# Kernel tuning notes

Hardware: AMD Instinct MI355X
Metric: run time of the kernel (lower is better)

Reference implementation:

```python
import jax, jax.numpy as jnp
import numpy as np

B, H, S, D = 2, 16, 2048, 64
MASK_NEG = 1e9


def setup_inputs() -> dict:
    key = jax.random.key(0)
    kq, kk, kv, km = jax.random.split(key, 4)
    Q = jax.random.normal(kq, (B, H, S, D), dtype=jnp.float32)
    K = jax.random.normal(kk, (B, H, S, D), dtype=jnp.float32)
    V = jax.random.normal(kv, (B, H, S, D), dtype=jnp.float32)
    # float 0/1 mask, broadcast over heads; 1 = masked-out position
    attn_mask = jax.random.randint(km, (B, 1, S, S), 0, 2).astype(jnp.float32)
    return {"Q": Q, "K": K, "V": V, "attn_mask": attn_mask}


def reference(Q, K, V, attn_mask):
    # scores: [B, H, S, S]
    attn_score = jnp.einsum('bhqd,bhkd->bhqk', Q, K)
    scale = jnp.sqrt(jnp.asarray(K.shape[-1], dtype=jnp.float32))
    attn_scale = attn_score / scale - MASK_NEG * attn_mask
    attn_prob = jax.nn.softmax(attn_scale, axis=-1)
    attn_out = jnp.einsum('bhqk,bhkd->bhqd', attn_prob, V)
    return attn_out
```

## Files before the change

kernel.cpp:

```cpp
#include <hip/hip_runtime.h>


#define S_LEN 2048
#define D_DIM 64
#define WPR   32
#define NIT   32

typedef __attribute__((ext_vector_type(8)))  short bf16x8;
typedef __attribute__((ext_vector_type(4)))  float f32x4;
typedef __attribute__((ext_vector_type(16))) float f32x16;
typedef unsigned uint2v __attribute__((ext_vector_type(2)));
typedef unsigned long long ull;

__device__ __forceinline__ f32x16 mfma32(bf16x8 a, bf16x8 b, f32x16 c) {
  return __builtin_amdgcn_mfma_f32_32x32x16_bf16(a, b, c, 0, 0, 0);
}
__device__ __forceinline__ f32x4 mfma16(bf16x8 a, bf16x8 b, f32x4 c) {
  return __builtin_amdgcn_mfma_f32_16x16x32_bf16(a, b, c, 0, 0, 0);
}
__device__ __forceinline__ unsigned short f2bf(float f) {
  unsigned u = __builtin_bit_cast(unsigned, f);
  unsigned r = u + 0x7FFFu + ((u >> 16) & 1u);
  return (unsigned short)(r >> 16);
}
__device__ __forceinline__ float bf2f(unsigned short s) {
  unsigned u = ((unsigned)s) << 16;
  return __builtin_bit_cast(float, u);
}
__device__ __forceinline__ unsigned packbf(float a, float b) {
  unsigned r;
  asm("v_cvt_pk_bf16_f32 %0, %1, %2" : "=v"(r) : "v"(a), "v"(b));
  return r;
}
__device__ __forceinline__ float fexp2(float x) {
#if __has_builtin(__builtin_amdgcn_exp2f)
  return __builtin_amdgcn_exp2f(x);
#else
  return exp2f(x);
#endif
}
__device__ __forceinline__ bool detect_bf16(const void* maskp) {
  const unsigned short* s = (const unsigned short*)maskp;
  unsigned short v = s[2 * (threadIdx.x & 63)];
  return __ballot(v == (unsigned short)0x3F80) != 0ull;
}
__device__ __forceinline__ int4 cvt_f8(const float* p) {
  float4 f0 = *(const float4*)p;
  float4 f1 = *(const float4*)(p + 4);
  int4 r;
  r.x = (int)packbf(f0.x, f0.y);
  r.y = (int)packbf(f0.z, f0.w);
  r.z = (int)packbf(f1.x, f1.y);
  r.w = (int)packbf(f1.z, f1.w);
  return r;
}
__device__ __forceinline__ void gl_lds16(const unsigned short* g, unsigned short* l) {
#if __has_builtin(__builtin_amdgcn_global_load_lds)
  __builtin_amdgcn_global_load_lds(
      (const __attribute__((address_space(1))) unsigned int*)g,
      (__attribute__((address_space(3))) unsigned int*)l, 16, 0, 0);
#else
  *(int4*)((char*)l + (threadIdx.x & 63) * 16) = *(const int4*)g;
#endif
}

#define C1 0.18033688011112042f
#define C2 1.4426950408889634e9f

#define SEG0 4096u
#define SEG1 2048u
#define SEG2 1024u
#define SEG3 2048u

__global__ __launch_bounds__(256) void prep_all(
    const void* __restrict__ M, const void* __restrict__ Kin,
    const void* __restrict__ Vin, const void* __restrict__ Qin,
    ull* __restrict__ bits, unsigned short* __restrict__ Kf,
    unsigned short* __restrict__ Vf, unsigned short* __restrict__ Qc) {
  __shared__ __align__(16) unsigned short T[64 * 72];
  const bool isb = detect_bf16(M);
  const unsigned bx = blockIdx.x;
  const int tid = threadIdx.x;

  if (bx < SEG0) {
    unsigned e0 = bx * 2048u + tid;
    #pragma unroll
    for (int j = 0; j < 8; ++j) {
      unsigned idx = e0 + (unsigned)j * 256u;
      bool on = isb ? (bf2f(((const unsigned short*)M)[idx]) > 0.5f)
                    : (((const float*)M)[idx] > 0.5f);
      ull bm = __ballot(on);
      if ((tid & 63) == 0) {
        unsigned c = idx & 2047u, r = (idx >> 11) & 2047u, bb = idx >> 22;
        bits[(((size_t)(bb * WPR + (c >> 6))) << 11) + r] = bm;
      }
    }
  } else if (bx < SEG0 + SEG1) {
    unsigned g = (bx - SEG0) * 256u + tid;
    unsigned lane = g & 63u, f = (g >> 6) & 7u, it = (g >> 9) & 31u, bh = g >> 14;
    unsigned t = f >> 2, dc = f & 3, hi = lane >> 5, l31 = lane & 31;
    size_t src = (size_t)bh * (S_LEN * D_DIM) +
                 (size_t)(it * 64 + t * 32 + l31) * D_DIM + dc * 16 + hi * 8;
    int4 out;
    if (isb) out = *(const int4*)((const unsigned short*)Kin + src);
    else     out = cvt_f8((const float*)Kin + src);
    *(int4*)&Kf[(size_t)g * 8] = out;
  } else if (bx < SEG0 + SEG1 + SEG2) {
    unsigned idx = bx - (SEG0 + SEG1);
    unsigned bh = idx >> 5, it = idx & 31u;
    {
      int k = tid >> 2, d0 = (tid & 3) * 16;
      size_t src = (size_t)bh * (S_LEN * D_DIM) + (size_t)(it * 64 + k) * D_DIM + d0;
      int4 a, c;
      if (isb) {
        const unsigned short* s = (const unsigned short*)Vin + src;
        a = *(const int4*)s; c = *(const int4*)(s + 8);
      } else {
        const float* s = (const float*)Vin + src;
        a = cvt_f8(s); c = cvt_f8(s + 8);
      }
      *(int4*)&T[k * 72 + d0] = a;
      *(int4*)&T[k * 72 + d0 + 8] = c;
    }
    __syncthreads();
    #pragma unroll
    for (int h = 0; h < 2; ++h) {
      int c = tid + h * 256;
      int lane = c & 63, f = c >> 6;
      int t = f >> 2, kc = (f >> 1) & 1, dt = f & 1;
      int hi = lane >> 5, l31 = lane & 31;
      unsigned short v[8];
      #pragma unroll
      for (int j = 0; j < 8; ++j)
        v[j] = T[(t * 32 + kc * 16 + hi * 8 + j) * 72 + dt * 32 + l31];
      *(int4*)&Vf[(((size_t)(bh * 32 + it)) * 8 + f) * 512 + lane * 8] = *(int4*)v;
    }
  } else {
    size_t i0 = ((size_t)(bx - (SEG0 + SEG1 + SEG2)) * 256 + tid) * 8;
    unsigned short v[8];
    if (isb) {
      *(int4*)v = *(const int4*)((const unsigned short*)Qin + i0);
      #pragma unroll
      for (int j = 0; j < 8; ++j) v[j] = f2bf(bf2f(v[j]) * C1);
    } else {
      const float* f = (const float*)Qin + i0;
      #pragma unroll
      for (int j = 0; j < 4; ++j)
        *((unsigned*)v + j) = packbf(f[2 * j] * C1, f[2 * j + 1] * C1);
    }
    *(int4*)&Qc[i0] = *(int4*)v;
  }
}

__global__ __launch_bounds__(256, 4) void attn_fast(
    const unsigned short* __restrict__ Qc, const unsigned short* __restrict__ Kf,
    const unsigned short* __restrict__ Vf, const ull* __restrict__ bits,
    const void* __restrict__ maskp, void* __restrict__ Op) {
  __shared__ __align__(16) unsigned short Stg[2][8][512];
  __shared__ float Ls[4][32];

  const bool isb = detect_bf16(maskp);
  const int tid  = threadIdx.x;
  const int wave = tid >> 6;
  const int lane = tid & 63;
  const int hi   = lane >> 5;
  const int l31  = lane & 31;
  const int id   = blockIdx.x;
  const int slot = id >> 3;
  const int bh   = (id & 7) * 4 + (slot & 3);
  const int qb   = slot >> 2;
  const int qbase = qb * 128 + wave * 32;
  const int b    = bh >> 4;
  const size_t base = (size_t)bh * S_LEN * D_DIM;
  const int xidx = ((lane ^ 32) & 63) * 4;

  bf16x8 qf[4];
  #pragma unroll
  for (int dc = 0; dc < 4; ++dc)
    qf[dc] = *(const bf16x8*)&Qc[base + (size_t)(qbase + l31) * D_DIM + dc * 16 + hi * 8];

  const unsigned short* Ksrc = Kf + (size_t)bh * 131072 + (size_t)wave * 512 + lane * 8;
  const unsigned short* Vsrc = Vf + (size_t)bh * 131072 + (size_t)wave * 512 + lane * 8;
  const size_t bitbase = ((size_t)(b * WPR) << 11) + (size_t)(qbase + l31);

  f32x16 acc_o[2];
  float ls0 = 0.f, ls1 = 0.f, ls2 = 0.f, ls3 = 0.f;
  #pragma unroll
  for (int r = 0; r < 16; ++r) { acc_o[0][r] = 0.f; acc_o[1][r] = 0.f; }

  gl_lds16(Ksrc, &Stg[0][wave][0]);
  gl_lds16(Vsrc, &Stg[0][4 + wave][0]);
  __syncthreads();

  ull wcur = 0;
  #pragma unroll 2
  for (int ks = 0; ks < 64; ++ks) {
    const int cur = ks & 1;
    if (ks < 63) {
      gl_lds16(Ksrc + (size_t)(ks + 1) * 2048, &Stg[cur ^ 1][wave][0]);
      gl_lds16(Vsrc + (size_t)(ks + 1) * 2048, &Stg[cur ^ 1][4 + wave][0]);
    }
    if (!(ks & 1)) wcur = bits[bitbase + ((size_t)(ks >> 1) << 11)];

    f32x16 sc;
    #pragma unroll
    for (int r = 0; r < 16; ++r) sc[r] = 0.f;
    #pragma unroll
    for (int dc = 0; dc < 4; ++dc) {
      bf16x8 kfr = *(const bf16x8*)&Stg[cur][dc][lane * 8];
      sc = mfma32(kfr, qf[dc], sc);
    }

    const unsigned wtv = (unsigned)((wcur >> (hi * 4)) >> (32 * (ks & 1)));

    float p[16];
    #pragma unroll
    for (int r = 0; r < 16; ++r) {
      float e = fexp2(sc[r]);
      unsigned bit = (wtv >> ((r & 3) + 8 * (r >> 2))) & 1u;
      p[r] = bit ? 0.0f : e;
    }
    ls0 += p[0] + p[4] + p[8]  + p[12];
    ls1 += p[1] + p[5] + p[9]  + p[13];
    ls2 += p[2] + p[6] + p[10] + p[14];
    ls3 += p[3] + p[7] + p[11] + p[15];

    #pragma unroll
    for (int kc = 0; kc < 2; ++kc) {
      unsigned pk0 = packbf(p[8 * kc + 0], p[8 * kc + 1]);
      unsigned pk1 = packbf(p[8 * kc + 2], p[8 * kc + 3]);
      unsigned pk2 = packbf(p[8 * kc + 4], p[8 * kc + 5]);
      unsigned pk3 = packbf(p[8 * kc + 6], p[8 * kc + 7]);
      uint4 d;
#if __has_builtin(__builtin_amdgcn_permlane32_swap)
      uint2v s02 = __builtin_amdgcn_permlane32_swap(pk0, pk2, false, false);
      uint2v s13 = __builtin_amdgcn_permlane32_swap(pk1, pk3, false, false);
      d.x = s02[0]; d.z = s02[1];
      d.y = s13[0]; d.w = s13[1];
#else
      unsigned x0 = (unsigned)__builtin_amdgcn_ds_bpermute(xidx, (int)pk0);
      unsigned x1 = (unsigned)__builtin_amdgcn_ds_bpermute(xidx, (int)pk1);
      unsigned x2 = (unsigned)__builtin_amdgcn_ds_bpermute(xidx, (int)pk2);
      unsigned x3 = (unsigned)__builtin_amdgcn_ds_bpermute(xidx, (int)pk3);
      d.x = hi ? x2 : pk0;
      d.y = hi ? x3 : pk1;
      d.z = hi ? pk2 : x0;
      d.w = hi ? pk3 : x1;
#endif
      bf16x8 pf = __builtin_bit_cast(bf16x8, d);
      #pragma unroll
      for (int dt = 0; dt < 2; ++dt) {
        bf16x8 vfr = *(const bf16x8*)&Stg[cur][4 + kc * 2 + dt][lane * 8];
        acc_o[dt] = mfma32(pf, vfr, acc_o[dt]);
      }
    }

    __syncthreads();
  }

  float lsum = (ls0 + ls1) + (ls2 + ls3);
  {
    int li = __builtin_bit_cast(int, lsum);
    float other = __builtin_bit_cast(float, __builtin_amdgcn_ds_bpermute(xidx, li));
    lsum += other;
  }
  if (hi == 0) Ls[wave][l31] = lsum;

  #pragma unroll
  for (int r = 0; r < 16; ++r) {
    int m = (r & 3) + 8 * (r >> 2) + 4 * hi;
    float inv = 1.0f / Ls[wave][m];
    float o0 = acc_o[0][r] * inv;
    float o1 = acc_o[1][r] * inv;
    size_t idx = base + (size_t)(qbase + m) * D_DIM + l31;
    if (isb) {
      ((unsigned short*)Op)[idx]      = f2bf(o0);
      ((unsigned short*)Op)[idx + 32] = f2bf(o1);
    } else {
      ((float*)Op)[idx]      = o0;
      ((float*)Op)[idx + 32] = o1;
    }
  }
}

__global__ __launch_bounds__(256, 2) void attn_fallback(
    const void* __restrict__ Qp, const void* __restrict__ Kp,
    const void* __restrict__ Vp, const void* __restrict__ maskp,
    void* __restrict__ Op) {
  __shared__ __align__(16) short QKlds[128 * 72];
  __shared__ __align__(16) short Vtlds[64 * 72];
  __shared__ __align__(16) short Plds2[128 * 72];

  const bool isb = detect_bf16(maskp);
  const int tid  = threadIdx.x;
  const int wave = tid >> 6;
  const int lane = tid & 63;
  const int l15  = lane & 15;
  const int quad = lane >> 4;
  const int q0   = blockIdx.x * 128;
  const int bh   = blockIdx.y;
  const int b    = bh >> 4;
  const size_t base = (size_t)bh * S_LEN * D_DIM;

  const short* Qs = (const short*)Qp; const float* Qf = (const float*)Qp;
  const short* Ks = (const short*)Kp; const float* Kf2 = (const float*)Kp;
  const short* Vs = (const short*)Vp; const float* Vf2 = (const float*)Vp;

  if (isb) {
    const short* Qg = Qs + base + (size_t)q0 * D_DIM;
    #pragma unroll
    for (int p = 0; p < 4; ++p) {
      int e = p * 2048 + tid * 8;
      *(int4*)&QKlds[(e >> 6) * 72 + (e & 63)] = *(const int4*)(Qg + e);
    }
  } else {
    const float* Qg = Qf + base + (size_t)q0 * D_DIM;
    #pragma unroll
    for (int p = 0; p < 4; ++p) {
      int e = p * 2048 + tid * 8;
      *(int4*)&QKlds[(e >> 6) * 72 + (e & 63)] = cvt_f8(Qg + e);
    }
  }
  __syncthreads();
  bf16x8 qf[2][2];
  #pragma unroll
  for (int mi = 0; mi < 2; ++mi)
    #pragma unroll
    for (int kt = 0; kt < 2; ++kt)
      qf[mi][kt] = *(const bf16x8*)&QKlds[(wave * 32 + mi * 16 + l15) * 72 + kt * 32 + quad * 8];
  __syncthreads();

  f32x4 acc_o[2][4];
  f32x4 acc_l[2];
  const f32x4 zero4 = {0.f, 0.f, 0.f, 0.f};
  #pragma unroll
  for (int mi = 0; mi < 2; ++mi) {
    acc_l[mi] = zero4;
    #pragma unroll
    for (int nt = 0; nt < 4; ++nt) acc_o[mi][nt] = zero4;
  }
  bf16x8 onesB;
  {
    short ov = (l15 == 0) ? (short)0x3F80 : (short)0;
    #pragma unroll
    for (int i = 0; i < 8; ++i) onesB[i] = ov;
  }

  for (int it = 0; it < NIT; ++it) {
    const int k0 = it * 64;
    if (isb) {
      const short* Kg = Ks + base + (size_t)k0 * D_DIM;
      #pragma unroll
      for (int p = 0; p < 2; ++p) {
        int e = p * 2048 + tid * 8;
        *(int4*)&QKlds[(e >> 6) * 72 + (e & 63)] = *(const int4*)(Kg + e);
      }
    } else {
      const float* Kg = Kf2 + base + (size_t)k0 * D_DIM;
      #pragma unroll
      for (int p = 0; p < 2; ++p) {
        int e = p * 2048 + tid * 8;
        *(int4*)&QKlds[(e >> 6) * 72 + (e & 63)] = cvt_f8(Kg + e);
      }
    }
    {
      const int r0 = (tid >> 3) * 2;
      const int d0 = (tid & 7) * 8;
      unsigned short as_[8], bs_[8];
      if (isb) {
        const short* Vg = Vs + base + (size_t)k0 * D_DIM;
        *(int4*)as_ = *(const int4*)(Vg + r0 * D_DIM + d0);
        *(int4*)bs_ = *(const int4*)(Vg + (r0 + 1) * D_DIM + d0);
      } else {
        const float* Vg = Vf2 + base + (size_t)k0 * D_DIM;
        *(int4*)as_ = cvt_f8(Vg + r0 * D_DIM + d0);
        *(int4*)bs_ = cvt_f8(Vg + (r0 + 1) * D_DIM + d0);
      }
      #pragma unroll
      for (int j = 0; j < 8; ++j) {
        int d = d0 + j;
        int blk = (r0 >> 3) ^ (d >> 3);
        unsigned pk = (unsigned)as_[j] | ((unsigned)bs_[j] << 16);
        *(unsigned*)&Vtlds[d * 72 + blk * 8 + (r0 & 7)] = pk;
      }
    }
    __syncthreads();

    f32x4 sc[2][4];
    #pragma unroll
    for (int mi = 0; mi < 2; ++mi)
      #pragma unroll
      for (int nt = 0; nt < 4; ++nt) sc[mi][nt] = zero4;
    #pragma unroll
    for (int nt = 0; nt < 4; ++nt) {
      bf16x8 kf0 = *(const bf16x8*)&QKlds[(nt * 16 + l15) * 72 + quad * 8];
      bf16x8 kf1 = *(const bf16x8*)&QKlds[(nt * 16 + l15) * 72 + 32 + quad * 8];
      #pragma unroll
      for (int mi = 0; mi < 2; ++mi) {
        sc[mi][nt] = mfma16(qf[mi][0], kf0, sc[mi][nt]);
        sc[mi][nt] = mfma16(qf[mi][1], kf1, sc[mi][nt]);
      }
    }

    #pragma unroll
    for (int mi = 0; mi < 2; ++mi) {
      #pragma unroll
      for (int nt = 0; nt < 4; ++nt) {
        #pragma unroll
        for (int reg = 0; reg < 4; ++reg) {
          int rg = q0 + wave * 32 + mi * 16 + quad * 4 + reg;
          size_t mix = (size_t)b * S_LEN * S_LEN + (size_t)rg * S_LEN + k0 + nt * 16 + l15;
          float mv = isb ? bf2f(((const unsigned short*)maskp)[mix])
                         : ((const float*)maskp)[mix];
          float y = sc[mi][nt][reg] * C1 - mv * C2;
          Plds2[(wave * 32 + mi * 16 + quad * 4 + reg) * 72 + nt * 16 + l15] =
              (short)f2bf(fexp2(y));
        }
      }
    }
    __syncthreads();

    #pragma unroll
    for (int kt = 0; kt < 2; ++kt) {
      bf16x8 pf[2];
      #pragma unroll
      for (int mi = 0; mi < 2; ++mi)
        pf[mi] = *(const bf16x8*)&Plds2[(wave * 32 + mi * 16 + l15) * 72 + kt * 32 + quad * 8];
      #pragma unroll
      for (int nt = 0; nt < 4; ++nt) {
        int d = nt * 16 + l15;
        int kb = (kt * 4 + quad) ^ (d >> 3);
        bf16x8 vf = *(const bf16x8*)&Vtlds[d * 72 + kb * 8];
        #pragma unroll
        for (int mi = 0; mi < 2; ++mi)
          acc_o[mi][nt] = mfma16(pf[mi], vf, acc_o[mi][nt]);
      }
      #pragma unroll
      for (int mi = 0; mi < 2; ++mi)
        acc_l[mi] = mfma16(pf[mi], onesB, acc_l[mi]);
    }
    __syncthreads();
  }

  #pragma unroll
  for (int mi = 0; mi < 2; ++mi) {
    #pragma unroll
    for (int reg = 0; reg < 4; ++reg) {
      float lv = __shfl(acc_l[mi][reg], lane & 48, 64);
      float inv = 1.0f / lv;
      #pragma unroll
      for (int nt = 0; nt < 4; ++nt) {
        float o = acc_o[mi][nt][reg] * inv;
        size_t idx = base + (size_t)(q0 + wave * 32 + mi * 16 + quad * 4 + reg) * D_DIM + nt * 16 + l15;
        if (isb) ((unsigned short*)Op)[idx] = f2bf(o);
        else     ((float*)Op)[idx] = o;
      }
    }
  }
}

extern "C" void kernel_launch(void* const* d_in, const int* in_sizes, int n_in,
                              void* d_out, int out_size, void* d_ws, size_t ws_size,
                              hipStream_t stream) {
  const void* Q = d_in[0];
  const void* K = d_in[1];
  const void* V = d_in[2];
  const void* M = d_in[3];

  dim3 block(256);
  const size_t bits_bytes = (size_t)2 * S_LEN * S_LEN / 8;
  const size_t tens_bytes = (size_t)2 * 16 * S_LEN * D_DIM * 2;

  if (ws_size >= bits_bytes + 3 * tens_bytes) {
    char* ws = (char*)d_ws;
    ull* bits = (ull*)ws;
    unsigned short* Kf = (unsigned short*)(ws + bits_bytes);
    unsigned short* Vf = (unsigned short*)(ws + bits_bytes + tens_bytes);
    unsigned short* Qc = (unsigned short*)(ws + bits_bytes + 2 * tens_bytes);
    prep_all<<<dim3(SEG0 + SEG1 + SEG2 + SEG3), block, 0, stream>>>(
        M, K, V, Q, bits, Kf, Vf, Qc);
    attn_fast<<<dim3(512), block, 0, stream>>>(Qc, Kf, Vf, bits, M, d_out);
  } else {
    attn_fallback<<<dim3(S_LEN / 128, 32), block, 0, stream>>>(Q, K, V, M, d_out);
  }
}
```

Measured before the change: 172.5 us.

## Process two key tiles per barrier with independent accumulators and halve occupancy

```diff
diff --git a/kernel.cpp b/kernel.cpp
--- a/kernel.cpp
+++ b/kernel.cpp
@@ -152,11 +152,11 @@
   }
 }
 
-__global__ __launch_bounds__(256, 4) void attn_fast(
+__global__ __launch_bounds__(256, 2) void attn_fast(
     const unsigned short* __restrict__ Qc, const unsigned short* __restrict__ Kf,
     const unsigned short* __restrict__ Vf, const ull* __restrict__ bits,
     const void* __restrict__ maskp, void* __restrict__ Op) {
-  __shared__ __align__(16) unsigned short Stg[2][8][512];
+  __shared__ __align__(16) unsigned short Stg[2][2][8][512];
   __shared__ float Ls[4][32];
 
   const bool isb = detect_bf16(maskp);
@@ -183,79 +183,122 @@
   const unsigned short* Vsrc = Vf + (size_t)bh * 131072 + (size_t)wave * 512 + lane * 8;
   const size_t bitbase = ((size_t)(b * WPR) << 11) + (size_t)(qbase + l31);
 
+  f32x16 accA[2], accB[2];
+  float ls0 = 0.f, ls1 = 0.f, ls2 = 0.f, ls3 = 0.f;
+  #pragma unroll
+  for (int r = 0; r < 16; ++r) {
+    accA[0][r] = 0.f; accA[1][r] = 0.f;
+    accB[0][r] = 0.f; accB[1][r] = 0.f;
+  }
+
+  #pragma unroll
+  for (int s = 0; s < 2; ++s) {
+    gl_lds16(Ksrc + (size_t)s * 2048, &Stg[0][s][wave][0]);
+    gl_lds16(Vsrc + (size_t)s * 2048, &Stg[0][s][4 + wave][0]);
+  }
+  ull wcur = bits[bitbase];
+  __syncthreads();
+
+  #pragma unroll 2
+  for (int f = 0; f < 32; ++f) {
+    const int cur = f & 1;
+    if (f < 31) {
+      #pragma unroll
+      for (int s = 0; s < 2; ++s) {
+        const size_t so = (size_t)(2 * (f + 1) + s) * 2048;
+        gl_lds16(Ksrc + so, &Stg[cur ^ 1][s][wave][0]);
+        gl_lds16(Vsrc + so, &Stg[cur ^ 1][s][4 + wave][0]);
+      }
+    }
+    ull wnext = (f < 31) ? bits[bitbase + ((size_t)(f + 1) << 11)] : 0ull;
+
+    bf16x8 ka[4], kb[4];
+    #pragma unroll
+    for (int dc = 0; dc < 4; ++dc) {
+      ka[dc] = *(const bf16x8*)&Stg[cur][0][dc][lane * 8];
+      kb[dc] = *(const bf16x8*)&Stg[cur][1][dc][lane * 8];
+    }
+    f32x16 scA, scB;
+    #pragma unroll
+    for (int r = 0; r < 16; ++r) { scA[r] = 0.f; scB[r] = 0.f; }
+    #pragma unroll
+    for (int dc = 0; dc < 4; ++dc) {
+      scA = mfma32(ka[dc], qf[dc], scA);
+      scB = mfma32(kb[dc], qf[dc], scB);
+    }
+
+    const ull wsh = wcur >> (hi * 4);
+    const unsigned wtvA = (unsigned)wsh;
+    const unsigned wtvB = (unsigned)(wsh >> 32);
+
+    float pA[16], pB[16];
+    #pragma unroll
+    for (int r = 0; r < 16; ++r) {
+      const int bi = (r & 3) + 8 * (r >> 2);
+      float eA = fexp2(scA[r]);
+      float eB = fexp2(scB[r]);
+      pA[r] = ((wtvA >> bi) & 1u) ? 0.0f : eA;
+      pB[r] = ((wtvB >> bi) & 1u) ? 0.0f : eB;
+    }
+    ls0 += (pA[0] + pA[4] + pA[8]  + pA[12]) + (pB[0] + pB[4] + pB[8]  + pB[12]);
+    ls1 += (pA[1] + pA[5] + pA[9]  + pA[13]) + (pB[1] + pB[5] + pB[9]  + pB[13]);
+    ls2 += (pA[2] + pA[6] + pA[10] + pA[14]) + (pB[2] + pB[6] + pB[10] + pB[14]);
+    ls3 += (pA[3] + pA[7] + pA[11] + pA[15]) + (pB[3] + pB[7] + pB[11] + pB[15]);
+
+    #pragma unroll
+    for (int kc = 0; kc < 2; ++kc) {
+      unsigned a0 = packbf(pA[8 * kc + 0], pA[8 * kc + 1]);
+      unsigned a1 = packbf(pA[8 * kc + 2], pA[8 * kc + 3]);
+      unsigned a2 = packbf(pA[8 * kc + 4], pA[8 * kc + 5]);
+      unsigned a3 = packbf(pA[8 * kc + 6], pA[8 * kc + 7]);
+      unsigned b0 = packbf(pB[8 * kc + 0], pB[8 * kc + 1]);
+      unsigned b1 = packbf(pB[8 * kc + 2], pB[8 * kc + 3]);
+      unsigned b2 = packbf(pB[8 * kc + 4], pB[8 * kc + 5]);
+      unsigned b3 = packbf(pB[8 * kc + 6], pB[8 * kc + 7]);
+      uint4 dA, dB;
+#if __has_builtin(__builtin_amdgcn_permlane32_swap)
+      uint2v sA02 = __builtin_amdgcn_permlane32_swap(a0, a2, false, false);
+      uint2v sA13 = __builtin_amdgcn_permlane32_swap(a1, a3, false, false);
+      dA.x = sA02[0]; dA.z = sA02[1];
+      dA.y = sA13[0]; dA.w = sA13[1];
+      uint2v sB02 = __builtin_amdgcn_permlane32_swap(b0, b2, false, false);
+      uint2v sB13 = __builtin_amdgcn_permlane32_swap(b1, b3, false, false);
+      dB.x = sB02[0]; dB.z = sB02[1];
+      dB.y = sB13[0]; dB.w = sB13[1];
+#else
+      unsigned xa0 = (unsigned)__builtin_amdgcn_ds_bpermute(xidx, (int)a0);
+      unsigned xa1 = (unsigned)__builtin_amdgcn_ds_bpermute(xidx, (int)a1);
+      unsigned xa2 = (unsigned)__builtin_amdgcn_ds_bpermute(xidx, (int)a2);
+      unsigned xa3 = (unsigned)__builtin_amdgcn_ds_bpermute(xidx, (int)a3);
+      dA.x = hi ? xa2 : a0;  dA.y = hi ? xa3 : a1;
+      dA.z = hi ? a2 : xa0;  dA.w = hi ? a3 : xa1;
+      unsigned xb0 = (unsigned)__builtin_amdgcn_ds_bpermute(xidx, (int)b0);
+      unsigned xb1 = (unsigned)__builtin_amdgcn_ds_bpermute(xidx, (int)b1);
+      unsigned xb2 = (unsigned)__builtin_amdgcn_ds_bpermute(xidx, (int)b2);
+      unsigned xb3 = (unsigned)__builtin_amdgcn_ds_bpermute(xidx, (int)b3);
+      dB.x = hi ? xb2 : b0;  dB.y = hi ? xb3 : b1;
+      dB.z = hi ? b2 : xb0;  dB.w = hi ? b3 : xb1;
+#endif
+      bf16x8 pfA = __builtin_bit_cast(bf16x8, dA);
+      bf16x8 pfB = __builtin_bit_cast(bf16x8, dB);
+      #pragma unroll
+      for (int dt = 0; dt < 2; ++dt) {
+        bf16x8 vfA = *(const bf16x8*)&Stg[cur][0][4 + kc * 2 + dt][lane * 8];
+        bf16x8 vfB = *(const bf16x8*)&Stg[cur][1][4 + kc * 2 + dt][lane * 8];
+        accA[dt] = mfma32(pfA, vfA, accA[dt]);
+        accB[dt] = mfma32(pfB, vfB, accB[dt]);
+      }
+    }
+
+    __syncthreads();
+    wcur = wnext;
+  }
+
   f32x16 acc_o[2];
-  float ls0 = 0.f, ls1 = 0.f, ls2 = 0.f, ls3 = 0.f;
-  #pragma unroll
-  for (int r = 0; r < 16; ++r) { acc_o[0][r] = 0.f; acc_o[1][r] = 0.f; }
-
-  gl_lds16(Ksrc, &Stg[0][wave][0]);
-  gl_lds16(Vsrc, &Stg[0][4 + wave][0]);
-  __syncthreads();
-
-  ull wcur = 0;
-  #pragma unroll 2
-  for (int ks = 0; ks < 64; ++ks) {
-    const int cur = ks & 1;
-    if (ks < 63) {
-      gl_lds16(Ksrc + (size_t)(ks + 1) * 2048, &Stg[cur ^ 1][wave][0]);
-      gl_lds16(Vsrc + (size_t)(ks + 1) * 2048, &Stg[cur ^ 1][4 + wave][0]);
-    }
-    if (!(ks & 1)) wcur = bits[bitbase + ((size_t)(ks >> 1) << 11)];
-
-    f32x16 sc;
-    #pragma unroll
-    for (int r = 0; r < 16; ++r) sc[r] = 0.f;
-    #pragma unroll
-    for (int dc = 0; dc < 4; ++dc) {
-      bf16x8 kfr = *(const bf16x8*)&Stg[cur][dc][lane * 8];
-      sc = mfma32(kfr, qf[dc], sc);
-    }
-
-    const unsigned wtv = (unsigned)((wcur >> (hi * 4)) >> (32 * (ks & 1)));
-
-    float p[16];
-    #pragma unroll
-    for (int r = 0; r < 16; ++r) {
-      float e = fexp2(sc[r]);
-      unsigned bit = (wtv >> ((r & 3) + 8 * (r >> 2))) & 1u;
-      p[r] = bit ? 0.0f : e;
-    }
-    ls0 += p[0] + p[4] + p[8]  + p[12];
-    ls1 += p[1] + p[5] + p[9]  + p[13];
-    ls2 += p[2] + p[6] + p[10] + p[14];
-    ls3 += p[3] + p[7] + p[11] + p[15];
-
-    #pragma unroll
-    for (int kc = 0; kc < 2; ++kc) {
-      unsigned pk0 = packbf(p[8 * kc + 0], p[8 * kc + 1]);
-      unsigned pk1 = packbf(p[8 * kc + 2], p[8 * kc + 3]);
-      unsigned pk2 = packbf(p[8 * kc + 4], p[8 * kc + 5]);
-      unsigned pk3 = packbf(p[8 * kc + 6], p[8 * kc + 7]);
-      uint4 d;
-#if __has_builtin(__builtin_amdgcn_permlane32_swap)
-      uint2v s02 = __builtin_amdgcn_permlane32_swap(pk0, pk2, false, false);
-      uint2v s13 = __builtin_amdgcn_permlane32_swap(pk1, pk3, false, false);
-      d.x = s02[0]; d.z = s02[1];
-      d.y = s13[0]; d.w = s13[1];
-#else
-      unsigned x0 = (unsigned)__builtin_amdgcn_ds_bpermute(xidx, (int)pk0);
-      unsigned x1 = (unsigned)__builtin_amdgcn_ds_bpermute(xidx, (int)pk1);
-      unsigned x2 = (unsigned)__builtin_amdgcn_ds_bpermute(xidx, (int)pk2);
-      unsigned x3 = (unsigned)__builtin_amdgcn_ds_bpermute(xidx, (int)pk3);
-      d.x = hi ? x2 : pk0;
-      d.y = hi ? x3 : pk1;
-      d.z = hi ? pk2 : x0;
-      d.w = hi ? pk3 : x1;
-#endif
-      bf16x8 pf = __builtin_bit_cast(bf16x8, d);
-      #pragma unroll
-      for (int dt = 0; dt < 2; ++dt) {
-        bf16x8 vfr = *(const bf16x8*)&Stg[cur][4 + kc * 2 + dt][lane * 8];
-        acc_o[dt] = mfma32(pf, vfr, acc_o[dt]);
-      }
-    }
-
-    __syncthreads();
+  #pragma unroll
+  for (int r = 0; r < 16; ++r) {
+    acc_o[0][r] = accA[0][r] + accB[0][r];
+    acc_o[1][r] = accA[1][r] + accB[1][r];
   }
 
   float lsum = (ls0 + ls1) + (ls2 + ls3);
```

Result: faster. 166.0 us (-3.8%).

## Split key range across wave pairs, compute row sums via MFMA

Applied to the files above, without the earlier changes.

```diff
diff --git a/kernel.cpp b/kernel.cpp
--- a/kernel.cpp
+++ b/kernel.cpp
@@ -156,8 +156,7 @@
     const unsigned short* __restrict__ Qc, const unsigned short* __restrict__ Kf,
     const unsigned short* __restrict__ Vf, const ull* __restrict__ bits,
     const void* __restrict__ maskp, void* __restrict__ Op) {
-  __shared__ __align__(16) unsigned short Stg[2][8][512];
-  __shared__ float Ls[4][32];
+  __shared__ __align__(16) unsigned short Stg[2][2][8][512];
 
   const bool isb = detect_bf16(maskp);
   const int tid  = threadIdx.x;
@@ -165,11 +164,13 @@
   const int lane = tid & 63;
   const int hi   = lane >> 5;
   const int l31  = lane & 31;
+  const int g    = wave >> 1;
+  const int rw   = wave & 1;
   const int id   = blockIdx.x;
   const int slot = id >> 3;
   const int bh   = (id & 7) * 4 + (slot & 3);
   const int qb   = slot >> 2;
-  const int qbase = qb * 128 + wave * 32;
+  const int qbase = qb * 64 + rw * 32;
   const int b    = bh >> 4;
   const size_t base = (size_t)bh * S_LEN * D_DIM;
   const int xidx = ((lane ^ 32) & 63) * 4;
@@ -179,39 +180,56 @@
   for (int dc = 0; dc < 4; ++dc)
     qf[dc] = *(const bf16x8*)&Qc[base + (size_t)(qbase + l31) * D_DIM + dc * 16 + hi * 8];
 
-  const unsigned short* Ksrc = Kf + (size_t)bh * 131072 + (size_t)wave * 512 + lane * 8;
-  const unsigned short* Vsrc = Vf + (size_t)bh * 131072 + (size_t)wave * 512 + lane * 8;
+  bf16x8 onesb;
+  #pragma unroll
+  for (int i = 0; i < 8; ++i) onesb[i] = (short)0x3F80;
+
+  const unsigned short* Kw = Kf + (size_t)bh * 131072 + (size_t)(2 * rw) * 512 + lane * 8;
+  const unsigned short* Vw = Vf + (size_t)bh * 131072 + (size_t)(2 * rw) * 512 + lane * 8;
+  const int ks0 = g * 32;
   const size_t bitbase = ((size_t)(b * WPR) << 11) + (size_t)(qbase + l31);
 
   f32x16 acc_o[2];
-  float ls0 = 0.f, ls1 = 0.f, ls2 = 0.f, ls3 = 0.f;
+  f32x16 acc_l;
+  f32x16 zv;
   #pragma unroll
-  for (int r = 0; r < 16; ++r) { acc_o[0][r] = 0.f; acc_o[1][r] = 0.f; }
-
-  gl_lds16(Ksrc, &Stg[0][wave][0]);
-  gl_lds16(Vsrc, &Stg[0][4 + wave][0]);
+  for (int r = 0; r < 16; ++r) {
+    acc_o[0][r] = 0.f; acc_o[1][r] = 0.f; acc_l[r] = 0.f; zv[r] = 0.f;
+  }
+
+  {
+    const size_t so = (size_t)ks0 * 2048;
+    gl_lds16(Kw + so,       &Stg[g][0][2 * rw][0]);
+    gl_lds16(Kw + so + 512, &Stg[g][0][2 * rw + 1][0]);
+    gl_lds16(Vw + so,       &Stg[g][0][4 + 2 * rw][0]);
+    gl_lds16(Vw + so + 512, &Stg[g][0][4 + 2 * rw + 1][0]);
+  }
   __syncthreads();
 
   ull wcur = 0;
   #pragma unroll 2
-  for (int ks = 0; ks < 64; ++ks) {
-    const int cur = ks & 1;
-    if (ks < 63) {
-      gl_lds16(Ksrc + (size_t)(ks + 1) * 2048, &Stg[cur ^ 1][wave][0]);
-      gl_lds16(Vsrc + (size_t)(ks + 1) * 2048, &Stg[cur ^ 1][4 + wave][0]);
-    }
-    if (!(ks & 1)) wcur = bits[bitbase + ((size_t)(ks >> 1) << 11)];
-
-    f32x16 sc;
-    #pragma unroll
-    for (int r = 0; r < 16; ++r) sc[r] = 0.f;
-    #pragma unroll
-    for (int dc = 0; dc < 4; ++dc) {
-      bf16x8 kfr = *(const bf16x8*)&Stg[cur][dc][lane * 8];
-      sc = mfma32(kfr, qf[dc], sc);
-    }
-
-    const unsigned wtv = (unsigned)((wcur >> (hi * 4)) >> (32 * (ks & 1)));
+  for (int f = 0; f < 32; ++f) {
+    const int cur = f & 1;
+    if (f < 31) {
+      const size_t so = (size_t)(ks0 + f + 1) * 2048;
+      gl_lds16(Kw + so,       &Stg[g][cur ^ 1][2 * rw][0]);
+      gl_lds16(Kw + so + 512, &Stg[g][cur ^ 1][2 * rw + 1][0]);
+      gl_lds16(Vw + so,       &Stg[g][cur ^ 1][4 + 2 * rw][0]);
+      gl_lds16(Vw + so + 512, &Stg[g][cur ^ 1][4 + 2 * rw + 1][0]);
+    }
+    if (!(f & 1)) wcur = bits[bitbase + ((size_t)(g * 16 + (f >> 1)) << 11)];
+
+    bf16x8 ka[4];
+    #pragma unroll
+    for (int dc = 0; dc < 4; ++dc)
+      ka[dc] = *(const bf16x8*)&Stg[g][cur][dc][lane * 8];
+    __builtin_amdgcn_s_setprio(1);
+    f32x16 sc = mfma32(ka[0], qf[0], zv);
+    #pragma unroll
+    for (int dc = 1; dc < 4; ++dc) sc = mfma32(ka[dc], qf[dc], sc);
+    __builtin_amdgcn_s_setprio(0);
+
+    const unsigned wtv = (unsigned)((wcur >> (hi * 4)) >> (32 * (f & 1)));
 
     float p[16];
     #pragma unroll
@@ -220,10 +238,6 @@
       unsigned bit = (wtv >> ((r & 3) + 8 * (r >> 2))) & 1u;
       p[r] = bit ? 0.0f : e;
     }
-    ls0 += p[0] + p[4] + p[8]  + p[12];
-    ls1 += p[1] + p[5] + p[9]  + p[13];
-    ls2 += p[2] + p[6] + p[10] + p[14];
-    ls3 += p[3] + p[7] + p[11] + p[15];
 
     #pragma unroll
     for (int kc = 0; kc < 2; ++kc) {
@@ -248,37 +262,45 @@
       d.w = hi ? pk3 : x1;
 #endif
       bf16x8 pf = __builtin_bit_cast(bf16x8, d);
+      __builtin_amdgcn_s_setprio(1);
       #pragma unroll
       for (int dt = 0; dt < 2; ++dt) {
-        bf16x8 vfr = *(const bf16x8*)&Stg[cur][4 + kc * 2 + dt][lane * 8];
+        bf16x8 vfr = *(const bf16x8*)&Stg[g][cur][4 + kc * 2 + dt][lane * 8];
         acc_o[dt] = mfma32(pf, vfr, acc_o[dt]);
       }
+      acc_l = mfma32(pf, onesb, acc_l);
+      __builtin_amdgcn_s_setprio(0);
     }
 
     __syncthreads();
   }
 
-  float lsum = (ls0 + ls1) + (ls2 + ls3);
-  {
-    int li = __builtin_bit_cast(int, lsum);
-    float other = __builtin_bit_cast(float, __builtin_amdgcn_ds_bpermute(xidx, li));
-    lsum += other;
-  }
-  if (hi == 0) Ls[wave][l31] = lsum;
-
-  #pragma unroll
-  for (int r = 0; r < 16; ++r) {
-    int m = (r & 3) + 8 * (r >> 2) + 4 * hi;
-    float inv = 1.0f / Ls[wave][m];
-    float o0 = acc_o[0][r] * inv;
-    float o1 = acc_o[1][r] * inv;
-    size_t idx = base + (size_t)(qbase + m) * D_DIM + l31;
-    if (isb) {
-      ((unsigned short*)Op)[idx]      = f2bf(o0);
-      ((unsigned short*)Op)[idx + 32] = f2bf(o1);
-    } else {
-      ((float*)Op)[idx]      = o0;
-      ((float*)Op)[idx + 32] = o1;
+  float* Cb = (float*)Stg;
+  if (g == 1) {
+    #pragma unroll
+    for (int r = 0; r < 16; ++r) {
+      Cb[(rw * 48 + r) * 64 + lane]      = acc_o[0][r];
+      Cb[(rw * 48 + 16 + r) * 64 + lane] = acc_o[1][r];
+      Cb[(rw * 48 + 32 + r) * 64 + lane] = acc_l[r];
+    }
+  }
+  __syncthreads();
+  if (g == 0) {
+    #pragma unroll
+    for (int r = 0; r < 16; ++r) {
+      float o0 = acc_o[0][r] + Cb[(rw * 48 + r) * 64 + lane];
+      float o1 = acc_o[1][r] + Cb[(rw * 48 + 16 + r) * 64 + lane];
+      float lv = acc_l[r]    + Cb[(rw * 48 + 32 + r) * 64 + lane];
+      int m = (r & 3) + 8 * (r >> 2) + 4 * hi;
+      float inv = 1.0f / lv;
+      size_t idx = base + (size_t)(qbase + m) * D_DIM + l31;
+      if (isb) {
+        ((unsigned short*)Op)[idx]      = f2bf(o0 * inv);
+        ((unsigned short*)Op)[idx + 32] = f2bf(o1 * inv);
+      } else {
+        ((float*)Op)[idx]      = o0 * inv;
+        ((float*)Op)[idx + 32] = o1 * inv;
+      }
     }
   }
 }
@@ -479,7 +501,7 @@
     unsigned short* Qc = (unsigned short*)(ws + bits_bytes + 2 * tens_bytes);
     prep_all<<<dim3(SEG0 + SEG1 + SEG2 + SEG3), block, 0, stream>>>(
         M, K, V, Q, bits, Kf, Vf, Qc);
-    attn_fast<<<dim3(512), block, 0, stream>>>(Qc, Kf, Vf, bits, M, d_out);
+    attn_fast<<<dim3(1024), block, 0, stream>>>(Qc, Kf, Vf, bits, M, d_out);
   } else {
     attn_fallback<<<dim3(S_LEN / 128, 32), block, 0, stream>>>(Q, K, V, M, d_out);
   }
```

After: 170.0 us. About the same (-1.5%).
